# Optimization experiments

Hardware: AMD Instinct MI355X
Metric: run time of the kernel (lower is better)

## Reference

```python
import jax, jax.numpy as jnp
import numpy as np

H = 192
W = 192
EPS = 1e-6


def _quat_to_rotmat(q):
    q = q / jnp.linalg.norm(q, axis=-1, keepdims=True)
    w, x, y, z = q[..., 0], q[..., 1], q[..., 2], q[..., 3]
    R = jnp.stack([
        1 - 2 * (y * y + z * z), 2 * (x * y - w * z), 2 * (x * z + w * y),
        2 * (x * y + w * z), 1 - 2 * (x * x + z * z), 2 * (y * z - w * x),
        2 * (x * z - w * y), 2 * (y * z + w * x), 1 - 2 * (x * x + y * y)],
        axis=-1)
    return R.reshape(q.shape[:-1] + (3, 3))


def _render(means, quats, scales, opacities, colors, betas, viewmats, Ks):
    B = viewmats.shape[0]
    N = means.shape[0]
    Rw = viewmats[:, :3, :3]                                  # [B,3,3]
    tw = viewmats[:, :3, 3]                                   # [B,3]
    # world -> camera
    p = jnp.einsum('bij,nj->bni', Rw, means) + tw[:, None, :]  # [B,N,3]
    # 3D covariance from quat + exp(scale): Sigma = M M^T, M = R_q diag(s)
    Rq = _quat_to_rotmat(quats)                                # [N,3,3]
    M = Rq * jnp.exp(scales)[:, None, :]
    cov3d = jnp.einsum('nij,nkj->nik', M, M)                   # [N,3,3]
    covc = jnp.einsum('bij,njk,blk->bnil', Rw, cov3d, Rw)      # [B,N,3,3]
    tx, ty = p[..., 0], p[..., 1]
    tz = jnp.maximum(p[..., 2], 1e-2)
    fx = Ks[:, 0, 0][:, None]
    fy = Ks[:, 1, 1][:, None]
    cx = Ks[:, 0, 2][:, None]
    cy = Ks[:, 1, 2][:, None]
    z1 = 1.0 / tz
    zero = jnp.zeros_like(tz)
    # perspective Jacobian [B,N,2,3]
    J = jnp.stack([
        jnp.stack([fx * z1, zero, -fx * tx * z1 * z1], axis=-1),
        jnp.stack([zero, fy * z1, -fy * ty * z1 * z1], axis=-1)], axis=-2)
    cov2d = jnp.einsum('bnij,bnjk,bnlk->bnil', J, covc, J)     # [B,N,2,2]
    a = cov2d[..., 0, 0] + 0.3                                 # screen-space blur (gsplat)
    b = cov2d[..., 0, 1]
    c = cov2d[..., 1, 1] + 0.3
    det = a * c - b * b
    u = fx * tx * z1 + cx
    v = fy * ty * z1 + cy
    # global front-to-back depth sort (non-packed reference)
    order = jnp.argsort(p[..., 2], axis=-1)                    # [B,N]

    def g(x):
        return jnp.take_along_axis(x, order, axis=1)

    u, v, a, b, c, det = g(u), g(v), g(a), g(b), g(c), g(det)
    tz_s = g(tz)
    op = g(jnp.broadcast_to(jax.nn.sigmoid(opacities)[None], (B, N)))
    bt = g(jnp.broadcast_to(betas[None], (B, N)))
    col = jnp.take_along_axis(
        jnp.broadcast_to(colors[None], (B, N, 3)),
        jnp.broadcast_to(order[..., None], (B, N, 3)), axis=1)
    inv_det = 1.0 / jnp.maximum(det, EPS)
    Ac = c * inv_det
    Bc = -b * inv_det
    Cc = a * inv_det
    xs = jnp.arange(W, dtype=jnp.float32) + 0.5
    ys = jnp.arange(H, dtype=jnp.float32) + 0.5
    dx = xs[None, None, :, None] - u[:, None, None, :]         # [B,H,W,N]
    dy = ys[None, :, None, None] - v[:, None, None, :]         # [B,H,W,N]
    sigma = 0.5 * (Ac[:, None, None, :] * dx * dx
                   + Cc[:, None, None, :] * dy * dy) \
            + Bc[:, None, None, :] * dx * dy
    sigma = jnp.maximum(sigma, 1e-8)
    # generalized-gaussian kernel with per-splat beta exponent
    alpha = op[:, None, None, :] * jnp.exp(-sigma ** bt[:, None, None, :])
    valid = (p[..., 2] > 1e-2)
    valid = jnp.take_along_axis(valid, order, axis=1) & (det > EPS)
    alpha = jnp.where(valid[:, None, None, :], alpha, 0.0)
    alpha = jnp.minimum(alpha, 0.999)
    alpha = jnp.where(alpha > 1.0 / 255.0, alpha, 0.0)
    T = jnp.cumprod(1.0 - alpha, axis=-1)
    T_excl = jnp.concatenate([jnp.ones_like(T[..., :1]), T[..., :-1]], axis=-1)
    w = alpha * T_excl                                         # [B,H,W,N]
    rgb = jnp.einsum('bhwn,bnc->bhwc', w, col)                 # [B,H,W,3]
    acc = jnp.sum(w, axis=-1)                                  # [B,H,W]
    return rgb, acc


def setup_inputs() -> dict:
    key = jax.random.key(0)
    ks = jax.random.split(key, 8)
    N = 512
    xy = (jax.random.uniform(ks[0], (N, 2)) - 0.5) * 4.0
    z = jax.random.uniform(ks[1], (N, 1)) * 6.0 + 2.0
    means = jnp.concatenate([xy, z], axis=1)
    quats = jax.random.normal(ks[2], (N, 4))
    scales = jax.random.normal(ks[3], (N, 3)) * 0.3 + np.log(0.05).astype(np.float32)
    opacities = jax.random.normal(ks[4], (N,))
    colors = jax.random.uniform(ks[5], (N, 3))
    betas = jnp.ones((N,), dtype=jnp.float32)
    viewmats = jnp.eye(4, dtype=jnp.float32)[None]
    Ks = jnp.array([[[220.0, 0.0, 96.0], [0.0, 220.0, 96.0], [0.0, 0.0, 1.0]]],
                   dtype=jnp.float32)
    return {'means': means, 'quats': quats, 'scales': scales,
            'opacities': opacities, 'colors': colors, 'betas': betas,
            'viewmats': viewmats, 'Ks': Ks}


def reference(means, quats, scales, opacities, colors, betas, viewmats, Ks):
    rgb, acc = _render(means, quats, scales, opacities, colors, betas,
                       viewmats, Ks)
    return rgb, acc
```

## Files before the change

### kernel.cpp

```cpp
#include <hip/hip_runtime.h>
#include <hip/hip_bf16.h>

#define NG 512
#define IMG_H 192
#define IMG_W 192
#define NPIX (IMG_H * IMG_W)
#define GF 12
#define NCHUNK 8

__global__ __launch_bounds__(512) void preprocess_kernel(
    const float* __restrict__ means, const float* __restrict__ quats,
    const float* __restrict__ scales, const float* __restrict__ opac,
    const float* __restrict__ colors, const float* __restrict__ betas,
    const float* __restrict__ vm, const float* __restrict__ Ks,
    float* __restrict__ ws)
{
    __shared__ __align__(16) float zsh[NG];
    __shared__ int rpart[4 * 128];

    const int tid = threadIdx.x;
    const int blk = blockIdx.x;
    const int gl  = tid & 127;
    const int seg = tid >> 7;
    const int g   = blk * 128 + gl;

    const float Rw[3][3] = {{vm[0], vm[1], vm[2]},
                            {vm[4], vm[5], vm[6]},
                            {vm[8], vm[9], vm[10]}};
    const float tw[3] = {vm[3], vm[7], vm[11]};
    const float fx = Ks[0], cx = Ks[2], fy = Ks[4], cy = Ks[5];

    {
        const float ax = means[tid*3+0], ay = means[tid*3+1], az = means[tid*3+2];
        zsh[tid] = Rw[2][0]*ax + Rw[2][1]*ay + Rw[2][2]*az + tw[2];
    }
    __syncthreads();

    const float zg = zsh[g];
    int cnt = 0;
    {
        const float4* z4 = (const float4*)(zsh + seg * 128);
        const int jbase = seg * 128;
        #pragma unroll 8
        for (int i = 0; i < 32; i++) {
            const float4 zz = z4[i];
            const int j = jbase + 4 * i;
            cnt += (zz.x < zg) || (zz.x == zg && (j + 0) < g);
            cnt += (zz.y < zg) || (zz.y == zg && (j + 1) < g);
            cnt += (zz.z < zg) || (zz.z == zg && (j + 2) < g);
            cnt += (zz.w < zg) || (zz.w == zg && (j + 3) < g);
        }
    }
    rpart[seg * 128 + gl] = cnt;
    __syncthreads();

    if (seg != 0) return;

    const int rank = rpart[gl] + rpart[128 + gl] + rpart[256 + gl] + rpart[384 + gl];

    const float mx = means[g*3+0], my = means[g*3+1], mz = means[g*3+2];
    const float px = Rw[0][0]*mx + Rw[0][1]*my + Rw[0][2]*mz + tw[0];
    const float py = Rw[1][0]*mx + Rw[1][1]*my + Rw[1][2]*mz + tw[1];
    const float pz = zg;

    float qw = quats[g*4+0], qx = quats[g*4+1], qy = quats[g*4+2], qz = quats[g*4+3];
    const float qn = 1.0f / sqrtf(qw*qw + qx*qx + qy*qy + qz*qz);
    qw *= qn; qx *= qn; qy *= qn; qz *= qn;
    float Rq[3][3];
    Rq[0][0] = 1.f - 2.f*(qy*qy + qz*qz); Rq[0][1] = 2.f*(qx*qy - qw*qz); Rq[0][2] = 2.f*(qx*qz + qw*qy);
    Rq[1][0] = 2.f*(qx*qy + qw*qz); Rq[1][1] = 1.f - 2.f*(qx*qx + qz*qz); Rq[1][2] = 2.f*(qy*qz - qw*qx);
    Rq[2][0] = 2.f*(qx*qz - qw*qy); Rq[2][1] = 2.f*(qy*qz + qw*qx); Rq[2][2] = 1.f - 2.f*(qx*qx + qy*qy);

    const float e0 = expf(scales[g*3+0]);
    const float e1 = expf(scales[g*3+1]);
    const float e2 = expf(scales[g*3+2]);

    float M[3][3];
    #pragma unroll
    for (int i = 0; i < 3; i++) { M[i][0] = Rq[i][0]*e0; M[i][1] = Rq[i][1]*e1; M[i][2] = Rq[i][2]*e2; }
    float c3[3][3];
    #pragma unroll
    for (int i = 0; i < 3; i++)
        #pragma unroll
        for (int k = 0; k < 3; k++)
            c3[i][k] = M[i][0]*M[k][0] + M[i][1]*M[k][1] + M[i][2]*M[k][2];

    float tmpm[3][3];
    #pragma unroll
    for (int i = 0; i < 3; i++)
        #pragma unroll
        for (int k = 0; k < 3; k++)
            tmpm[i][k] = Rw[i][0]*c3[0][k] + Rw[i][1]*c3[1][k] + Rw[i][2]*c3[2][k];
    float S[3][3];
    #pragma unroll
    for (int i = 0; i < 3; i++)
        #pragma unroll
        for (int l = 0; l < 3; l++)
            S[i][l] = tmpm[i][0]*Rw[l][0] + tmpm[i][1]*Rw[l][1] + tmpm[i][2]*Rw[l][2];

    const float tz = fmaxf(pz, 0.01f);
    const float z1 = 1.0f / tz;
    const float j0 = fx*z1, j2 = -fx*px*z1*z1;
    const float j1 = fy*z1, j3 = -fy*py*z1*z1;

    const float cov00 = j0*j0*S[0][0] + 2.f*j0*j2*S[0][2] + j2*j2*S[2][2];
    const float cov01 = j0*j1*S[0][1] + j0*j3*S[0][2] + j2*j1*S[1][2] + j2*j3*S[2][2];
    const float cov11 = j1*j1*S[1][1] + 2.f*j1*j3*S[1][2] + j3*j3*S[2][2];

    const float a = cov00 + 0.3f;
    const float b = cov01;
    const float c = cov11 + 0.3f;
    const float det = a*c - b*b;
    const float u = fx*px*z1 + cx;
    const float v = fy*py*z1 + cy;
    const bool valid = (pz > 0.01f) && (det > 1e-6f);
    const float inv_det = 1.0f / fmaxf(det, 1e-6f);
    float op = 1.0f / (1.0f + expf(-opac[g]));
    if (!valid) op = 0.0f;

    float* dst = ws + rank * GF;
    dst[0]  = u;  dst[1] = v;
    dst[2]  = c * inv_det;
    dst[3]  = -b * inv_det;
    dst[4]  = a * inv_det;
    dst[5]  = op; dst[6] = betas[g];
    dst[7]  = colors[g*3+0]; dst[8] = colors[g*3+1]; dst[9] = colors[g*3+2];
    dst[10] = 0.0f; dst[11] = 0.0f;
}

__global__ __launch_bounds__(512) void render_kernel(
    const float* __restrict__ ws, float* __restrict__ out)
{
    __shared__ __align__(16) float gs[NG * GF];
    __shared__ int clist[NG];
    __shared__ float part[NCHUNK * 64 * 5];
    __shared__ int wcnt[NCHUNK];
    __shared__ int woff[NCHUNK + 1];

    const int tid  = threadIdx.x;
    const int lane = tid & 63;
    const int wv   = tid >> 6;

    {
        const float4* src = (const float4*)ws;
        float4* dst = (float4*)gs;
        #pragma unroll
        for (int i = 0; i < NG * GF / 4 / 512; i++)
            dst[tid + i * 512] = src[tid + i * 512];
    }
    __syncthreads();

    const int strip = blockIdx.x;
    const int y  = strip / 3;
    const int x0 = (strip % 3) * 64;
    const float fyp = (float)y + 0.5f;
    const float xlo = (float)x0 + 0.5f;
    const float xhi = (float)x0 + 63.5f;

    {
        const float* gp = gs + tid * GF;
        const float u = gp[0], v = gp[1], A = gp[2], B = gp[3], C = gp[4];
        const float op = gp[5], bt = gp[6];
        const float dy = fyp - v;
        const float dxlo = xlo - u, dxhi = xhi - u;
        float dxs = -B * dy / fmaxf(A, 1e-12f);
        dxs = fminf(fmaxf(dxs, dxlo), dxhi);
        float smin = 0.5f * (A * dxs * dxs + C * dy * dy) + B * dxs * dy;
        smin = fmaxf(smin, 1e-8f);
        const float se = (bt == 1.0f) ? smin : powf(smin, bt);
        const float amax = op * expf(-se);
        const bool keep = amax > (1.0f / 255.0f);

        const unsigned long long m = __ballot(keep);
        if (lane == 0) wcnt[wv] = __popcll(m);
        __syncthreads();
        if (tid == 0) {
            int s = 0;
            #pragma unroll
            for (int k = 0; k < NCHUNK; k++) { woff[k] = s; s += wcnt[k]; }
            woff[NCHUNK] = s;
        }
        __syncthreads();
        if (keep) {
            const int pos = woff[wv] + __popcll(m & ((1ULL << lane) - 1));
            clist[pos] = tid;
        }
    }
    __syncthreads();

    const int total = woff[NCHUNK];
    const int s = (wv * total) >> 3;
    const int e = ((wv + 1) * total) >> 3;

    const float fxp = (float)(x0 + lane) + 0.5f;
    float T = 1.0f, cr = 0.0f, cg = 0.0f, cb = 0.0f, ac = 0.0f;
    for (int i = s; i < e; i++) {
        const float* gp = gs + clist[i] * GF;
        const float dx = fxp - gp[0];
        const float dy = fyp - gp[1];
        float sigma = 0.5f * (gp[2]*dx*dx + gp[4]*dy*dy) + gp[3]*dx*dy;
        sigma = fmaxf(sigma, 1e-8f);
        const float bt = gp[6];
        const float se = (bt == 1.0f) ? sigma : powf(sigma, bt);
        float alpha = gp[5] * expf(-se);
        alpha = fminf(alpha, 0.999f);
        if (!(alpha > (1.0f / 255.0f))) alpha = 0.0f;
        const float w = alpha * T;
        cr += w * gp[7]; cg += w * gp[8]; cb += w * gp[9];
        ac += w;
        T *= 1.0f - alpha;
    }

    float* pp = part + (wv * 64 + lane) * 5;
    pp[0] = cr; pp[1] = cg; pp[2] = cb; pp[3] = ac; pp[4] = T;
    __syncthreads();

    if (wv == 0) {
        float Tt = 1.0f, r = 0.0f, g = 0.0f, b = 0.0f, a = 0.0f;
        #pragma unroll
        for (int k = 0; k < NCHUNK; k++) {
            const float* pk = part + (k * 64 + lane) * 5;
            r += Tt * pk[0]; g += Tt * pk[1]; b += Tt * pk[2]; a += Tt * pk[3];
            Tt *= pk[4];
        }
        const int pix = y * IMG_W + x0 + lane;
        out[pix * 3 + 0] = r;
        out[pix * 3 + 1] = g;
        out[pix * 3 + 2] = b;
        out[NPIX * 3 + pix] = a;
    }
}

extern "C" void kernel_launch(void* const* d_in, const int* in_sizes, int n_in,
                              void* d_out, int out_size, void* d_ws, size_t ws_size,
                              hipStream_t stream) {
    const float* means  = (const float*)d_in[0];
    const float* quats  = (const float*)d_in[1];
    const float* scales = (const float*)d_in[2];
    const float* opac   = (const float*)d_in[3];
    const float* colors = (const float*)d_in[4];
    const float* betas  = (const float*)d_in[5];
    const float* vm     = (const float*)d_in[6];
    const float* Ks     = (const float*)d_in[7];
    float* ws  = (float*)d_ws;
    float* out = (float*)d_out;

    preprocess_kernel<<<4, 512, 0, stream>>>(means, quats, scales, opac, colors, betas, vm, Ks, ws);
    render_kernel<<<NPIX / 64, 512, 0, stream>>>(ws, out);
}
```

Measured before the change: 74.61 us.

## Fuse preprocessing into tiled render kernel with per-tile culling and sort

Merges the two kernels into one. Each 64x8 tile block redundantly preprocesses all 512 gaussians, culls them against the tile rectangle using a bound on the conic's minimum over the tile, then depth-sorts only the survivors by rank-counting in shared memory. Each wave renders one pixel row sequentially over the sorted list, which removes the per-wave chunk split and the compositing merge. In exchange the preprocessing work is repeated in every block and each pixel walks the whole survivor list serially.

```diff
diff --git a/kernel.cpp b/kernel.cpp
--- a/kernel.cpp
+++ b/kernel.cpp
@@ -1,69 +1,57 @@
 #include <hip/hip_runtime.h>
-#include <hip/hip_bf16.h>
 
 #define NG 512
 #define IMG_H 192
 #define IMG_W 192
 #define NPIX (IMG_H * IMG_W)
 #define GF 12
-#define NCHUNK 8
-
-__global__ __launch_bounds__(512) void preprocess_kernel(
+#define TILE_W 64
+#define TILE_H 8
+#define GX (IMG_W / TILE_W)
+#define GY (IMG_H / TILE_H)
+
+__global__ __launch_bounds__(512) void splat_fused(
     const float* __restrict__ means, const float* __restrict__ quats,
     const float* __restrict__ scales, const float* __restrict__ opac,
     const float* __restrict__ colors, const float* __restrict__ betas,
     const float* __restrict__ vm, const float* __restrict__ Ks,
-    float* __restrict__ ws)
+    float* __restrict__ out)
 {
-    __shared__ __align__(16) float zsh[NG];
-    __shared__ int rpart[4 * 128];
-
-    const int tid = threadIdx.x;
-    const int blk = blockIdx.x;
-    const int gl  = tid & 127;
-    const int seg = tid >> 7;
-    const int g   = blk * 128 + gl;
-
-    const float Rw[3][3] = {{vm[0], vm[1], vm[2]},
-                            {vm[4], vm[5], vm[6]},
-                            {vm[8], vm[9], vm[10]}};
-    const float tw[3] = {vm[3], vm[7], vm[11]};
-    const float fx = Ks[0], cx = Ks[2], fy = Ks[4], cy = Ks[5];
-
-    {
-        const float ax = means[tid*3+0], ay = means[tid*3+1], az = means[tid*3+2];
-        zsh[tid] = Rw[2][0]*ax + Rw[2][1]*ay + Rw[2][2]*az + tw[2];
-    }
-    __syncthreads();
-
-    const float zg = zsh[g];
-    int cnt = 0;
-    {
-        const float4* z4 = (const float4*)(zsh + seg * 128);
-        const int jbase = seg * 128;
-        #pragma unroll 8
-        for (int i = 0; i < 32; i++) {
-            const float4 zz = z4[i];
-            const int j = jbase + 4 * i;
-            cnt += (zz.x < zg) || (zz.x == zg && (j + 0) < g);
-            cnt += (zz.y < zg) || (zz.y == zg && (j + 1) < g);
-            cnt += (zz.z < zg) || (zz.z == zg && (j + 2) < g);
-            cnt += (zz.w < zg) || (zz.w == zg && (j + 3) < g);
-        }
-    }
-    rpart[seg * 128 + gl] = cnt;
-    __syncthreads();
-
-    if (seg != 0) return;
-
-    const int rank = rpart[gl] + rpart[128 + gl] + rpart[256 + gl] + rpart[384 + gl];
-
-    const float mx = means[g*3+0], my = means[g*3+1], mz = means[g*3+2];
-    const float px = Rw[0][0]*mx + Rw[0][1]*my + Rw[0][2]*mz + tw[0];
-    const float py = Rw[1][0]*mx + Rw[1][1]*my + Rw[1][2]*mz + tw[1];
-    const float pz = zg;
-
-    float qw = quats[g*4+0], qx = quats[g*4+1], qy = quats[g*4+2], qz = quats[g*4+3];
+    __shared__ __align__(16) float gs[NG * GF];
+    __shared__ unsigned long long skey[NG];
+    __shared__ int wcnt[8];
+    __shared__ int woff[9];
+
+    const int tid  = threadIdx.x;
+    const int lane = tid & 63;
+    const int wv   = tid >> 6;
+
+    const int bx = blockIdx.x % GX;
+    const int by = blockIdx.x / GX;
+    const int x0 = bx * TILE_W;
+    const int y0 = by * TILE_H;
+
+    const float mx = means[tid*3+0], my = means[tid*3+1], mz = means[tid*3+2];
+    const float4 q4 = *(const float4*)(quats + tid*4);
+    const float s0 = scales[tid*3+0], s1 = scales[tid*3+1], s2 = scales[tid*3+2];
+    const float opraw = opac[tid];
+    const float col0 = colors[tid*3+0], col1 = colors[tid*3+1], col2 = colors[tid*3+2];
+    const float bt = betas[tid];
+
+    const float Rw00=vm[0], Rw01=vm[1], Rw02=vm[2],  tw0=vm[3];
+    const float Rw10=vm[4], Rw11=vm[5], Rw12=vm[6],  tw1=vm[7];
+    const float Rw20=vm[8], Rw21=vm[9], Rw22=vm[10], tw2=vm[11];
+    const float fx=Ks[0], cx=Ks[2], fy=Ks[4], cy=Ks[5];
+
+    const float px_ = Rw00*mx + Rw01*my + Rw02*mz + tw0;
+    const float py_ = Rw10*mx + Rw11*my + Rw12*mz + tw1;
+    const float pz  = Rw20*mx + Rw21*my + Rw22*mz + tw2;
+
+    unsigned int ub = __float_as_uint(pz);
+    ub = (pz < 0.0f) ? ~ub : (ub | 0x80000000u);
+    const unsigned long long kd = ((unsigned long long)ub << 32) | (unsigned int)tid;
+
+    float qw = q4.x, qx = q4.y, qy = q4.z, qz = q4.w;
     const float qn = 1.0f / sqrtf(qw*qw + qx*qx + qy*qy + qz*qz);
     qw *= qn; qx *= qn; qy *= qn; qz *= qn;
     float Rq[3][3];
@@ -71,9 +59,7 @@
     Rq[1][0] = 2.f*(qx*qy + qw*qz); Rq[1][1] = 1.f - 2.f*(qx*qx + qz*qz); Rq[1][2] = 2.f*(qy*qz - qw*qx);
     Rq[2][0] = 2.f*(qx*qz - qw*qy); Rq[2][1] = 2.f*(qy*qz + qw*qx); Rq[2][2] = 1.f - 2.f*(qx*qx + qy*qy);
 
-    const float e0 = expf(scales[g*3+0]);
-    const float e1 = expf(scales[g*3+1]);
-    const float e2 = expf(scales[g*3+2]);
+    const float e0 = expf(s0), e1 = expf(s1), e2 = expf(s2);
 
     float M[3][3];
     #pragma unroll
@@ -85,6 +71,7 @@
         for (int k = 0; k < 3; k++)
             c3[i][k] = M[i][0]*M[k][0] + M[i][1]*M[k][1] + M[i][2]*M[k][2];
 
+    const float Rw[3][3] = {{Rw00,Rw01,Rw02},{Rw10,Rw11,Rw12},{Rw20,Rw21,Rw22}};
     float tmpm[3][3];
     #pragma unroll
     for (int i = 0; i < 3; i++)
@@ -100,8 +87,8 @@
 
     const float tz = fmaxf(pz, 0.01f);
     const float z1 = 1.0f / tz;
-    const float j0 = fx*z1, j2 = -fx*px*z1*z1;
-    const float j1 = fy*z1, j3 = -fy*py*z1*z1;
+    const float j0 = fx*z1, j2 = -fx*px_*z1*z1;
+    const float j1 = fy*z1, j3 = -fy*py_*z1*z1;
 
     const float cov00 = j0*j0*S[0][0] + 2.f*j0*j2*S[0][2] + j2*j2*S[2][2];
     const float cov01 = j0*j1*S[0][1] + j0*j3*S[0][2] + j2*j1*S[1][2] + j2*j3*S[2][2];
@@ -111,129 +98,99 @@
     const float b = cov01;
     const float c = cov11 + 0.3f;
     const float det = a*c - b*b;
-    const float u = fx*px*z1 + cx;
-    const float v = fy*py*z1 + cy;
+    const float uu = fx*px_*z1 + cx;
+    const float vv = fy*py_*z1 + cy;
     const bool valid = (pz > 0.01f) && (det > 1e-6f);
     const float inv_det = 1.0f / fmaxf(det, 1e-6f);
-    float op = 1.0f / (1.0f + expf(-opac[g]));
+    const float Ac = c * inv_det;
+    const float Bc = -b * inv_det;
+    const float Cc = a * inv_det;
+    float op = 1.0f / (1.0f + expf(-opraw));
     if (!valid) op = 0.0f;
 
-    float* dst = ws + rank * GF;
-    dst[0]  = u;  dst[1] = v;
-    dst[2]  = c * inv_det;
-    dst[3]  = -b * inv_det;
-    dst[4]  = a * inv_det;
-    dst[5]  = op; dst[6] = betas[g];
-    dst[7]  = colors[g*3+0]; dst[8] = colors[g*3+1]; dst[9] = colors[g*3+2];
-    dst[10] = 0.0f; dst[11] = 0.0f;
-}
-
-__global__ __launch_bounds__(512) void render_kernel(
-    const float* __restrict__ ws, float* __restrict__ out)
-{
-    __shared__ __align__(16) float gs[NG * GF];
-    __shared__ int clist[NG];
-    __shared__ float part[NCHUNK * 64 * 5];
-    __shared__ int wcnt[NCHUNK];
-    __shared__ int woff[NCHUNK + 1];
-
-    const int tid  = threadIdx.x;
-    const int lane = tid & 63;
-    const int wv   = tid >> 6;
-
-    {
-        const float4* src = (const float4*)ws;
-        float4* dst = (float4*)gs;
-        #pragma unroll
-        for (int i = 0; i < NG * GF / 4 / 512; i++)
-            dst[tid + i * 512] = src[tid + i * 512];
-    }
-    __syncthreads();
-
-    const int strip = blockIdx.x;
-    const int y  = strip / 3;
-    const int x0 = (strip % 3) * 64;
-    const float fyp = (float)y + 0.5f;
-    const float xlo = (float)x0 + 0.5f;
-    const float xhi = (float)x0 + 63.5f;
-
-    {
-        const float* gp = gs + tid * GF;
-        const float u = gp[0], v = gp[1], A = gp[2], B = gp[3], C = gp[4];
-        const float op = gp[5], bt = gp[6];
-        const float dy = fyp - v;
-        const float dxlo = xlo - u, dxhi = xhi - u;
-        float dxs = -B * dy / fmaxf(A, 1e-12f);
-        dxs = fminf(fmaxf(dxs, dxlo), dxhi);
-        float smin = 0.5f * (A * dxs * dxs + C * dy * dy) + B * dxs * dy;
-        smin = fmaxf(smin, 1e-8f);
-        const float se = (bt == 1.0f) ? smin : powf(smin, bt);
-        const float amax = op * expf(-se);
-        const bool keep = amax > (1.0f / 255.0f);
-
-        const unsigned long long m = __ballot(keep);
-        if (lane == 0) wcnt[wv] = __popcll(m);
-        __syncthreads();
-        if (tid == 0) {
-            int s = 0;
-            #pragma unroll
-            for (int k = 0; k < NCHUNK; k++) { woff[k] = s; s += wcnt[k]; }
-            woff[NCHUNK] = s;
-        }
-        __syncthreads();
-        if (keep) {
-            const int pos = woff[wv] + __popcll(m & ((1ULL << lane) - 1));
-            clist[pos] = tid;
-        }
-    }
-    __syncthreads();
-
-    const int total = woff[NCHUNK];
-    const int s = (wv * total) >> 3;
-    const int e = ((wv + 1) * total) >> 3;
+    const float xlo = (float)x0 + 0.5f, xhi = (float)x0 + (float)TILE_W - 0.5f;
+    const float ylo = (float)y0 + 0.5f, yhi = (float)y0 + (float)TILE_H - 0.5f;
+    const float dxl = xlo - uu, dxh = xhi - uu;
+    const float dyl = ylo - vv, dyh = yhi - vv;
+    float smin = 0.0f;
+    if (!(dxl <= 0.0f && dxh >= 0.0f && dyl <= 0.0f && dyh >= 0.0f)) {
+        const float rA = 1.0f / Ac, rC = 1.0f / Cc;
+        float dxs, dys;
+        dxs = fminf(fmaxf(-Bc*dyl*rA, dxl), dxh);
+        const float s1e = 0.5f*(Ac*dxs*dxs + Cc*dyl*dyl) + Bc*dxs*dyl;
+        dxs = fminf(fmaxf(-Bc*dyh*rA, dxl), dxh);
+        const float s2e = 0.5f*(Ac*dxs*dxs + Cc*dyh*dyh) + Bc*dxs*dyh;
+        dys = fminf(fmaxf(-Bc*dxl*rC, dyl), dyh);
+        const float s3e = 0.5f*(Ac*dxl*dxl + Cc*dys*dys) + Bc*dxl*dys;
+        dys = fminf(fmaxf(-Bc*dxh*rC, dyl), dyh);
+        const float s4e = 0.5f*(Ac*dxh*dxh + Cc*dys*dys) + Bc*dxh*dys;
+        smin = fmaxf(fminf(fminf(s1e, s2e), fminf(s3e, s4e)), 0.0f);
+    }
+    const float smc  = fmaxf(smin, 1e-8f);
+    const float sem  = (bt == 1.0f) ? smc : powf(smc, bt);
+    const float amax = op * expf(-sem);
+    const bool keep  = amax > (1.0f / 255.0f);
+
+    const unsigned long long bal = __ballot(keep);
+    if (lane == 0) wcnt[wv] = __popcll(bal);
+    __syncthreads();
+    if (tid == 0) {
+        int sacc = 0;
+        #pragma unroll
+        for (int k = 0; k < 8; k++) { woff[k] = sacc; sacc += wcnt[k]; }
+        woff[8] = sacc;
+    }
+    __syncthreads();
+    if (keep) {
+        const int p = woff[wv] + __popcll(bal & ((1ULL << lane) - 1));
+        skey[p] = kd;
+    }
+    __syncthreads();
+
+    const int total = woff[8];
+
+    if (keep) {
+        int rs = 0;
+        for (int j = 0; j < total; j++) rs += (skey[j] < kd) ? 1 : 0;
+        float4* dst = (float4*)(gs + rs * GF);
+        dst[0] = make_float4(uu, vv, Ac, Bc);
+        dst[1] = make_float4(Cc, op, bt, col0);
+        dst[2] = make_float4(col1, col2, 0.0f, 0.0f);
+    }
+    __syncthreads();
 
     const float fxp = (float)(x0 + lane) + 0.5f;
-    float T = 1.0f, cr = 0.0f, cg = 0.0f, cb = 0.0f, ac = 0.0f;
-    for (int i = s; i < e; i++) {
-        const float* gp = gs + clist[i] * GF;
-        const float dx = fxp - gp[0];
-        const float dy = fyp - gp[1];
-        float sigma = 0.5f * (gp[2]*dx*dx + gp[4]*dy*dy) + gp[3]*dx*dy;
+    const float fyp = (float)(y0 + wv)  + 0.5f;
+    float T = 1.0f, cr = 0.0f, cg = 0.0f, cb = 0.0f, acw = 0.0f;
+    for (int i = 0; i < total; i++) {
+        const float4 r0 = *(const float4*)(gs + i*GF);
+        const float4 r1 = *(const float4*)(gs + i*GF + 4);
+        const float2 r2 = *(const float2*)(gs + i*GF + 8);
+        const float dx = fxp - r0.x;
+        const float dy = fyp - r0.y;
+        float sigma = 0.5f*(r0.z*dx*dx + r1.x*dy*dy) + r0.w*dx*dy;
         sigma = fmaxf(sigma, 1e-8f);
-        const float bt = gp[6];
-        const float se = (bt == 1.0f) ? sigma : powf(sigma, bt);
-        float alpha = gp[5] * expf(-se);
+        const float se = (r1.z == 1.0f) ? sigma : powf(sigma, r1.z);
+        float alpha = r1.y * expf(-se);
         alpha = fminf(alpha, 0.999f);
         if (!(alpha > (1.0f / 255.0f))) alpha = 0.0f;
         const float w = alpha * T;
-        cr += w * gp[7]; cg += w * gp[8]; cb += w * gp[9];
-        ac += w;
+        cr += w * r1.w; cg += w * r2.x; cb += w * r2.y;
+        acw += w;
         T *= 1.0f - alpha;
     }
 
-    float* pp = part + (wv * 64 + lane) * 5;
-    pp[0] = cr; pp[1] = cg; pp[2] = cb; pp[3] = ac; pp[4] = T;
-    __syncthreads();
-
-    if (wv == 0) {
-        float Tt = 1.0f, r = 0.0f, g = 0.0f, b = 0.0f, a = 0.0f;
-        #pragma unroll
-        for (int k = 0; k < NCHUNK; k++) {
-            const float* pk = part + (k * 64 + lane) * 5;
-            r += Tt * pk[0]; g += Tt * pk[1]; b += Tt * pk[2]; a += Tt * pk[3];
-            Tt *= pk[4];
-        }
-        const int pix = y * IMG_W + x0 + lane;
-        out[pix * 3 + 0] = r;
-        out[pix * 3 + 1] = g;
-        out[pix * 3 + 2] = b;
-        out[NPIX * 3 + pix] = a;
-    }
+    const int pix = (y0 + wv) * IMG_W + x0 + lane;
+    out[pix*3 + 0] = cr;
+    out[pix*3 + 1] = cg;
+    out[pix*3 + 2] = cb;
+    out[NPIX*3 + pix] = acw;
 }
 
 extern "C" void kernel_launch(void* const* d_in, const int* in_sizes, int n_in,
                               void* d_out, int out_size, void* d_ws, size_t ws_size,
                               hipStream_t stream) {
+    (void)in_sizes; (void)n_in; (void)d_ws; (void)ws_size; (void)out_size;
     const float* means  = (const float*)d_in[0];
     const float* quats  = (const float*)d_in[1];
     const float* scales = (const float*)d_in[2];
@@ -242,9 +199,7 @@
     const float* betas  = (const float*)d_in[5];
     const float* vm     = (const float*)d_in[6];
     const float* Ks     = (const float*)d_in[7];
-    float* ws  = (float*)d_ws;
     float* out = (float*)d_out;
 
-    preprocess_kernel<<<4, 512, 0, stream>>>(means, quats, scales, opac, colors, betas, vm, Ks, ws);
-    render_kernel<<<NPIX / 64, 512, 0, stream>>>(ws, out);
+    splat_fused<<<GX * GY, 512, 0, stream>>>(means, quats, scales, opac, colors, betas, vm, Ks, out);
 }
```

Result: no change. 75.97 us (+1.8%).
